# Kernel tuning notes

Hardware: AMD Instinct MI355X
Metric: run time of the kernel (lower is better)

Reference implementation:

```python
import jax, jax.numpy as jnp
import numpy as np

# Adaptive spatial attention with visual sentinel (Lu et al., 'Knowing When to Look').
# k = 49 spatial regions (7x7), d = 2048 feature channels.
# Scores: z_l = w_h . tanh(W_v v_l + W_g h_t)  per region l
#         s  = w_h_s . tanh(W_s s_t + W_g h_t) sentinel score
# softmax over [z_1..z_49, s] -> (alpha, beta); c_t = sum_l alpha_l v_l
# output = beta * s_t + (1 - beta) * c_t + h_t

B, K_REG, D = 2048, 49, 2048
INIT = 0.05  # keras 'uniform' initializer range


def setup_inputs() -> dict:
    key = jax.random.key(0)
    ks = jax.random.split(key, 8)
    return {
        "V": jax.random.normal(ks[0], (B, K_REG, D), jnp.float32),
        "h_t": jax.random.normal(ks[1], (B, D), jnp.float32),
        "s_t": jax.random.normal(ks[2], (B, D), jnp.float32),
        "W_v": jax.random.uniform(ks[3], (K_REG, D), jnp.float32, -INIT, INIT),
        "W_g": jax.random.uniform(ks[4], (K_REG, D), jnp.float32, -INIT, INIT),
        "W_s": jax.random.uniform(ks[5], (K_REG, D), jnp.float32, -INIT, INIT),
        "w_h": jax.random.uniform(ks[6], (K_REG,), jnp.float32, -INIT, INIT),
        "w_h_s": jax.random.uniform(ks[7], (K_REG,), jnp.float32, -INIT, INIT),
    }


def reference(V, h_t, s_t, W_v, W_g, W_s, w_h, w_h_s):
    # (B, L=49 regions, K=49 hidden)
    W_vV = jnp.einsum('bld,kd->blk', V, W_v)
    W_gt = h_t @ W_g.T                               # (B, K)
    z_t = jnp.einsum('blk,k->bl', jnp.tanh(W_vV + W_gt[:, None, :]), w_h)   # (B, L)
    sent = jnp.einsum('bk,k->b', jnp.tanh(s_t @ W_s.T + W_gt), w_h_s)        # (B,)
    logits = jnp.concatenate([z_t, sent[:, None]], axis=1)                   # (B, L+1)
    a = jax.nn.softmax(logits, axis=-1)
    alpha, beta = a[:, :-1], a[:, -1:]               # (B,L), (B,1)
    c_t = jnp.einsum('bl,bld->bd', alpha, V)         # (B, D)
    return beta * s_t + (1.0 - beta) * c_t + h_t
```

## Files before the change

kernel.cpp:

```cpp
#include <hip/hip_runtime.h>
#include <hip/hip_bf16.h>

#define BATCH 2048
#define DIM   2048
#define KR    49
#define KC    64
#define LSTR  72

typedef __attribute__((ext_vector_type(8))) short short8;
typedef __attribute__((ext_vector_type(4))) float float4v;

__device__ __forceinline__ unsigned short f2b(float x) {
    __hip_bfloat16 h = __float2bfloat16(x);
    return __builtin_bit_cast(unsigned short, h);
}

__global__ __launch_bounds__(256) void precompute_kernel(
    const float* __restrict__ h_t, const float* __restrict__ s_t,
    const float* __restrict__ W_v, const float* __restrict__ W_g,
    const float* __restrict__ W_s, const float* __restrict__ w_h_s,
    float* __restrict__ Wgt, float* __restrict__ Ts,
    unsigned short* __restrict__ Wvb)
{
    const int idx = blockIdx.x * 256 + threadIdx.x;
    if (idx >= BATCH * KR) return;
    Wvb[idx] = f2b(W_v[idx]);
    const int b = idx / KR;
    const int k = idx - b * KR;
    const float4* h4 = (const float4*)(h_t + (size_t)b * DIM);
    const float4* s4 = (const float4*)(s_t + (size_t)b * DIM);
    const float4* g4 = (const float4*)(W_g + (size_t)k * DIM);
    const float4* w4 = (const float4*)(W_s + (size_t)k * DIM);
    float ag = 0.f, as = 0.f;
    #pragma unroll 4
    for (int d = 0; d < DIM / 4; ++d) {
        float4 hv = h4[d], gv = g4[d];
        ag += hv.x * gv.x + hv.y * gv.y + hv.z * gv.z + hv.w * gv.w;
        float4 sv = s4[d], wv = w4[d];
        as += sv.x * wv.x + sv.y * wv.y + sv.z * wv.z + sv.w * wv.w;
    }
    Wgt[idx] = ag;
    Ts[idx]  = tanhf(as + ag) * w_h_s[k];
}

__global__ __launch_bounds__(256) void fused_kernel(
    const float* __restrict__ V, const float* __restrict__ h_t,
    const float* __restrict__ s_t, const float* __restrict__ w_h,
    const float* __restrict__ Wgt, const float* __restrict__ Ts,
    const unsigned short* __restrict__ Wvb, float* __restrict__ out)
{
    const int b    = blockIdx.x;
    const int tid  = threadIdx.x;
    const int wave = tid >> 6;
    const int lane = tid & 63;
    const int quad = lane >> 4;
    const int l16  = lane & 15;

    __shared__ unsigned short Av[64 * LSTR];
    __shared__ unsigned short Bw[64 * LSTR];
    __shared__ float z_lds[64];
    __shared__ float alpha_l[KR];
    __shared__ float wgt_l[KR];
    __shared__ float wh_l[KR];
    __shared__ float beta_sh;

    if (tid < KR) {
        wgt_l[tid] = Wgt[(size_t)b * KR + tid];
        wh_l[tid]  = w_h[tid];
    }
    for (int i = tid; i < 15 * LSTR; i += 256) {
        Av[49 * LSTR + i] = 0;
        Bw[49 * LSTR + i] = 0;
    }

    float4v acc[4];
    #pragma unroll
    for (int t = 0; t < 4; ++t) acc[t] = (float4v){0.f, 0.f, 0.f, 0.f};

    const float* Vb = V + (size_t)b * KR * DIM;

    for (int kc = 0; kc < DIM; kc += KC) {
        for (int e = tid; e < KR * (KC / 4); e += 256) {
            const int row = e >> 4;
            const int c4  = e & 15;
            float4 v = *(const float4*)(Vb + (size_t)row * DIM + kc + c4 * 4);
            ushort4 pv;
            pv.x = f2b(v.x); pv.y = f2b(v.y); pv.z = f2b(v.z); pv.w = f2b(v.w);
            *(ushort4*)&Av[row * LSTR + c4 * 4] = pv;
            ushort4 wv = *(const ushort4*)(Wvb + (size_t)row * DIM + kc + c4 * 4);
            *(ushort4*)&Bw[row * LSTR + c4 * 4] = wv;
        }
        __syncthreads();
        const unsigned short* ap = &Av[(wave * 16 + l16) * LSTR + quad * 8];
        #pragma unroll
        for (int s = 0; s < 2; ++s) {
            short8 af = *(const short8*)(ap + s * 32);
            #pragma unroll
            for (int t = 0; t < 4; ++t) {
                short8 bf = *(const short8*)(&Bw[(t * 16 + l16) * LSTR + quad * 8 + s * 32]);
                acc[t] = __builtin_amdgcn_mfma_f32_16x16x32_bf16(af, bf, acc[t], 0, 0, 0);
            }
        }
        __syncthreads();
    }

    float zp[4] = {0.f, 0.f, 0.f, 0.f};
    #pragma unroll
    for (int t = 0; t < 4; ++t) {
        const int col = t * 16 + l16;
        if (col < KR) {
            const float wg = wgt_l[col];
            const float wh = wh_l[col];
            #pragma unroll
            for (int r = 0; r < 4; ++r)
                zp[r] += tanhf(acc[t][r] + wg) * wh;
        }
    }
    #pragma unroll
    for (int off = 1; off < 16; off <<= 1) {
        #pragma unroll
        for (int r = 0; r < 4; ++r)
            zp[r] += __shfl_xor(zp[r], off, 64);
    }
    if (l16 == 0) {
        #pragma unroll
        for (int r = 0; r < 4; ++r) {
            const int row = wave * 16 + quad * 4 + r;
            if (row < KR) z_lds[row] = zp[r];
        }
    }
    __syncthreads();

    if (wave == 0) {
        float tv = (lane < KR) ? Ts[(size_t)b * KR + lane] : 0.f;
        float sent = tv;
        #pragma unroll
        for (int off = 1; off < 64; off <<= 1) sent += __shfl_xor(sent, off, 64);
        float x = (lane < KR) ? z_lds[lane] : ((lane == KR) ? sent : -1e30f);
        float m = x;
        #pragma unroll
        for (int off = 1; off < 64; off <<= 1) m = fmaxf(m, __shfl_xor(m, off, 64));
        float e = (lane <= KR) ? expf(x - m) : 0.f;
        float s = e;
        #pragma unroll
        for (int off = 1; off < 64; off <<= 1) s += __shfl_xor(s, off, 64);
        const float a = e / s;
        if (lane < KR) alpha_l[lane] = a;
        if (lane == KR) beta_sh = a;
    }
    __syncthreads();

    const float bta = beta_sh;
    const float omb = 1.f - bta;
    const float4* h4 = (const float4*)(h_t + (size_t)b * DIM);
    const float4* s4 = (const float4*)(s_t + (size_t)b * DIM);
    float4* o4 = (float4*)(out + (size_t)b * DIM);
    for (int d4 = tid; d4 < DIM / 4; d4 += 256) {
        const float4* vp = (const float4*)Vb + d4;
        float ax = 0.f, ay = 0.f, az = 0.f, aw = 0.f;
        #pragma unroll 7
        for (int l = 0; l < KR; ++l) {
            const float al = alpha_l[l];
            float4 v = vp[(size_t)l * (DIM / 4)];
            ax += al * v.x; ay += al * v.y; az += al * v.z; aw += al * v.w;
        }
        float4 hv = h4[d4], sv = s4[d4], o;
        o.x = bta * sv.x + omb * ax + hv.x;
        o.y = bta * sv.y + omb * ay + hv.y;
        o.z = bta * sv.z + omb * az + hv.z;
        o.w = bta * sv.w + omb * aw + hv.w;
        o4[d4] = o;
    }
}

extern "C" void kernel_launch(void* const* d_in, const int* in_sizes, int n_in,
                              void* d_out, int out_size, void* d_ws, size_t ws_size,
                              hipStream_t stream) {
    const float* V     = (const float*)d_in[0];
    const float* h_t   = (const float*)d_in[1];
    const float* s_t   = (const float*)d_in[2];
    const float* W_v   = (const float*)d_in[3];
    const float* W_g   = (const float*)d_in[4];
    const float* W_s   = (const float*)d_in[5];
    const float* w_h   = (const float*)d_in[6];
    const float* w_h_s = (const float*)d_in[7];
    float* out = (float*)d_out;

    float* Wgt = (float*)d_ws;
    float* Ts  = Wgt + (size_t)BATCH * KR;
    unsigned short* Wvb = (unsigned short*)(Ts + (size_t)BATCH * KR);

    hipLaunchKernelGGL(precompute_kernel, dim3((BATCH * KR) / 256), dim3(256), 0, stream,
                       h_t, s_t, W_v, W_g, W_s, w_h_s, Wgt, Ts, Wvb);
    hipLaunchKernelGGL(fused_kernel, dim3(BATCH), dim3(256), 0, stream,
                       V, h_t, s_t, w_h, Wgt, Ts, Wvb, out);
}
```

Before: 1.581 ms.

## Load MFMA operands directly from global memory, dropping LDS staging and barriers

The score GEMM no longer stages V and W_v tiles through shared memory with two barriers per K-chunk. Each lane now loads its A fragment straight from global V, converting with a cheap truncating bf16 pack, and its B fragment straight from the bf16 W_v copy. Padding rows are handled by clamping row indices and zeroing the w_h weights for padded columns. This trades LDS traffic and synchronisation for redundant global/L2 reads of W_v across waves, and truncation in place of round-to-nearest. It also fixes the precompute grid size to cover all elements.

```diff
diff --git a/kernel.cpp b/kernel.cpp
--- a/kernel.cpp
+++ b/kernel.cpp
@@ -5,7 +5,6 @@
 #define DIM   2048
 #define KR    49
 #define KC    64
-#define LSTR  72
 
 typedef __attribute__((ext_vector_type(8))) short short8;
 typedef __attribute__((ext_vector_type(4))) float float4v;
@@ -13,6 +12,12 @@
 __device__ __forceinline__ unsigned short f2b(float x) {
     __hip_bfloat16 h = __float2bfloat16(x);
     return __builtin_bit_cast(unsigned short, h);
+}
+
+__device__ __forceinline__ unsigned int pack2_trunc(float lo, float hi) {
+    unsigned int a = __builtin_bit_cast(unsigned int, lo);
+    unsigned int b = __builtin_bit_cast(unsigned int, hi);
+    return (b & 0xffff0000u) | (a >> 16);
 }
 
 __global__ __launch_bounds__(256) void precompute_kernel(
@@ -56,65 +61,67 @@
     const int quad = lane >> 4;
     const int l16  = lane & 15;
 
-    __shared__ unsigned short Av[64 * LSTR];
-    __shared__ unsigned short Bw[64 * LSTR];
     __shared__ float z_lds[64];
     __shared__ float alpha_l[KR];
-    __shared__ float wgt_l[KR];
-    __shared__ float wh_l[KR];
+    __shared__ float wgt_l[64];
+    __shared__ float wh_l[64];
     __shared__ float beta_sh;
 
     if (tid < KR) {
         wgt_l[tid] = Wgt[(size_t)b * KR + tid];
         wh_l[tid]  = w_h[tid];
-    }
-    for (int i = tid; i < 15 * LSTR; i += 256) {
-        Av[49 * LSTR + i] = 0;
-        Bw[49 * LSTR + i] = 0;
+    } else if (tid < 64) {
+        wgt_l[tid] = 0.f;
+        wh_l[tid]  = 0.f;
+    }
+    __syncthreads();
+
+    const float* Vb = V + (size_t)b * KR * DIM;
+
+    const int arow = min(wave * 16 + l16, KR - 1);
+    const float* aBase = Vb + (size_t)arow * DIM + quad * 8;
+
+    const unsigned short* bBase[4];
+    #pragma unroll
+    for (int t = 0; t < 4; ++t) {
+        const int brow = min(t * 16 + l16, KR - 1);
+        bBase[t] = Wvb + (size_t)brow * DIM + quad * 8;
     }
 
     float4v acc[4];
     #pragma unroll
     for (int t = 0; t < 4; ++t) acc[t] = (float4v){0.f, 0.f, 0.f, 0.f};
 
-    const float* Vb = V + (size_t)b * KR * DIM;
-
+    #pragma unroll 2
     for (int kc = 0; kc < DIM; kc += KC) {
-        for (int e = tid; e < KR * (KC / 4); e += 256) {
-            const int row = e >> 4;
-            const int c4  = e & 15;
-            float4 v = *(const float4*)(Vb + (size_t)row * DIM + kc + c4 * 4);
-            ushort4 pv;
-            pv.x = f2b(v.x); pv.y = f2b(v.y); pv.z = f2b(v.z); pv.w = f2b(v.w);
-            *(ushort4*)&Av[row * LSTR + c4 * 4] = pv;
-            ushort4 wv = *(const ushort4*)(Wvb + (size_t)row * DIM + kc + c4 * 4);
-            *(ushort4*)&Bw[row * LSTR + c4 * 4] = wv;
-        }
-        __syncthreads();
-        const unsigned short* ap = &Av[(wave * 16 + l16) * LSTR + quad * 8];
         #pragma unroll
         for (int s = 0; s < 2; ++s) {
-            short8 af = *(const short8*)(ap + s * 32);
+            const float* ap = aBase + kc + s * 32;
+            float4 v0 = *(const float4*)ap;
+            float4 v1 = *(const float4*)(ap + 4);
+            uint4 p;
+            p.x = pack2_trunc(v0.x, v0.y);
+            p.y = pack2_trunc(v0.z, v0.w);
+            p.z = pack2_trunc(v1.x, v1.y);
+            p.w = pack2_trunc(v1.z, v1.w);
+            short8 af = __builtin_bit_cast(short8, p);
             #pragma unroll
             for (int t = 0; t < 4; ++t) {
-                short8 bf = *(const short8*)(&Bw[(t * 16 + l16) * LSTR + quad * 8 + s * 32]);
+                short8 bf = *(const short8*)(bBase[t] + kc + s * 32);
                 acc[t] = __builtin_amdgcn_mfma_f32_16x16x32_bf16(af, bf, acc[t], 0, 0, 0);
             }
         }
-        __syncthreads();
     }
 
     float zp[4] = {0.f, 0.f, 0.f, 0.f};
     #pragma unroll
     for (int t = 0; t < 4; ++t) {
         const int col = t * 16 + l16;
-        if (col < KR) {
-            const float wg = wgt_l[col];
-            const float wh = wh_l[col];
-            #pragma unroll
-            for (int r = 0; r < 4; ++r)
-                zp[r] += tanhf(acc[t][r] + wg) * wh;
-        }
+        const float wg = wgt_l[col];
+        const float wh = wh_l[col];
+        #pragma unroll
+        for (int r = 0; r < 4; ++r)
+            zp[r] += tanhf(acc[t][r] + wg) * wh;
     }
     #pragma unroll
     for (int off = 1; off < 16; off <<= 1) {
@@ -190,7 +197,7 @@
     float* Ts  = Wgt + (size_t)BATCH * KR;
     unsigned short* Wvb = (unsigned short*)(Ts + (size_t)BATCH * KR);
 
-    hipLaunchKernelGGL(precompute_kernel, dim3((BATCH * KR) / 256), dim3(256), 0, stream,
+    hipLaunchKernelGGL(precompute_kernel, dim3((BATCH * KR + 255) / 256), dim3(256), 0, stream,
                        h_t, s_t, W_v, W_g, W_s, w_h_s, Wgt, Ts, Wvb);
     hipLaunchKernelGGL(fused_kernel, dim3(BATCH), dim3(256), 0, stream,
                        V, h_t, s_t, w_h, Wgt, Ts, Wvb, out);
```

After: 1.537 ms. 1.03x faster.
